# Kernel tuning notes

Hardware: AMD Instinct MI355X
Metric: run time of the kernel (lower is better)

Reference implementation:

```python
import jax, jax.numpy as jnp
import numpy as np

NUM_HEADS = 16
HEAD_SIZE = 256
HIDDEN = NUM_HEADS * HEAD_SIZE  # 4096
ROTARY_DIM = 64
TOTAL_TOKENS = 8192
BATCH = 8
NUM_SLOTS = 16384


def setup_inputs() -> dict:
    key = jax.random.key(0)
    ks = jax.random.split(key, 6)
    hidden_states = jax.random.normal(ks[0], (TOTAL_TOKENS, HIDDEN), dtype=jnp.float32)
    w_qkv = jax.random.normal(ks[1], (3 * HIDDEN, HIDDEN), dtype=jnp.float32) * 0.02
    w_o = jax.random.normal(ks[2], (HIDDEN, HIDDEN), dtype=jnp.float32) * 0.02
    # cos/sin per token for the first rotary_dim dims (rotary_dim//2 freqs)
    cos = jax.random.uniform(ks[3], (TOTAL_TOKENS, ROTARY_DIM // 2), dtype=jnp.float32)
    sin = jax.random.uniform(ks[4], (TOTAL_TOKENS, ROTARY_DIM // 2), dtype=jnp.float32)
    key_cache = jnp.zeros((NUM_SLOTS, NUM_HEADS, HEAD_SIZE), dtype=jnp.float32)
    value_cache = jnp.zeros((NUM_SLOTS, NUM_HEADS, HEAD_SIZE), dtype=jnp.float32)
    slots = jnp.arange(TOTAL_TOKENS, dtype=jnp.int64) if jax.config.jax_enable_x64 else jnp.arange(TOTAL_TOKENS, dtype=jnp.int32)
    return {
        "hidden_states": hidden_states, "w_qkv": w_qkv, "w_o": w_o,
        "cos": cos, "sin": sin,
        "key_cache": key_cache, "value_cache": value_cache,
        "slots": slots, "batch_size": BATCH,
    }


def _apply_rope(x, cos, sin, rotary_dim):
    # x: [T, H, D]; rotate-half applied only to the first rotary_dim dims
    half = rotary_dim // 2
    x1 = x[..., :half]
    x2 = x[..., half:rotary_dim]
    c = cos[:, None, :]  # [T, 1, half]
    s = sin[:, None, :]
    rot = jnp.concatenate([x1 * c - x2 * s, x2 * c + x1 * s], axis=-1)
    return jnp.concatenate([rot, x[..., rotary_dim:]], axis=-1)


def reference(hidden_states, w_qkv, w_o, cos, sin, key_cache, value_cache, slots, batch_size):
    T, H = hidden_states.shape
    nh, hd = key_cache.shape[1], key_cache.shape[2]
    rotary_dim = 2 * cos.shape[1]
    scale = float(hd) ** -0.5

    # fused QKV projection (no bias), then split
    qkv = hidden_states @ w_qkv.T  # [T, 3H]
    q, k, v = jnp.split(qkv, 3, axis=1)
    q = q.reshape(T, nh, hd)
    k = k.reshape(T, nh, hd)
    v = v.reshape(T, nh, hd)

    # partial rotary embedding on first rotary_dim dims
    q = _apply_rope(q, cos, sin, rotary_dim)
    k = _apply_rope(k, cos, sin, rotary_dim)

    # KV-cache slot scatter, then gather back (prefill reads what was stored)
    key_cache = key_cache.at[slots].set(k)
    value_cache = value_cache.at[slots].set(v)
    k = key_cache[slots]
    v = value_cache[slots]

    # prefill flash-attention path: equal-length sequences, causal per sequence
    B = batch_size
    S = T // B
    qb = q.reshape(B, S, nh, hd)
    kb = k.reshape(B, S, nh, hd)
    vb = v.reshape(B, S, nh, hd)

    scores = jnp.einsum('bqhd,bkhd->bhqk', qb, kb) * scale  # [B, nh, S, S]
    causal = jnp.tril(jnp.ones((S, S), dtype=bool))
    scores = jnp.where(causal[None, None], scores, jnp.finfo(scores.dtype).min)
    attn = jax.nn.softmax(scores, axis=-1)
    out = jnp.einsum('bhqk,bkhd->bqhd', attn, vb).reshape(T, nh * hd)

    return out @ w_o.T
```

## Files before the change

### kernel.cpp

```cpp
#include <hip/hip_runtime.h>
#include <stdint.h>


typedef __bf16 bf16x8 __attribute__((ext_vector_type(8)));
typedef float f32x4 __attribute__((ext_vector_type(4)));

__device__ __forceinline__ unsigned short f2bf(float f) {
    union { float f; unsigned int u; } x;
    x.f = f;
    unsigned int r = x.u + 0x7fffu + ((x.u >> 16) & 1u);
    return (unsigned short)(r >> 16);
}

__device__ __forceinline__ float bf2f(unsigned short h) {
    union { unsigned int u; float f; } x;
    x.u = ((unsigned int)h) << 16;
    return x.f;
}

__device__ __forceinline__ void gld16(const void* g, void* l) {
    __builtin_amdgcn_global_load_lds(
        (const __attribute__((address_space(1))) void*)g,
        (__attribute__((address_space(3))) void*)l, 16, 0, 0);
}

__global__ __launch_bounds__(256) void cvt_bf16(const float* __restrict__ src,
                                                unsigned short* __restrict__ dst,
                                                long n4) {
    long i = (long)blockIdx.x * 256 + threadIdx.x;
    long stride = (long)gridDim.x * 256;
    for (; i < n4; i += stride) {
        float4 v = ((const float4*)src)[i];
        ushort4 o;
        o.x = f2bf(v.x); o.y = f2bf(v.y); o.z = f2bf(v.z); o.w = f2bf(v.w);
        ((ushort4*)dst)[i] = o;
    }
}

template <int EPI>
__global__ __launch_bounds__(256) void gemm_bt(
    const unsigned short* __restrict__ A, long astride, long abatch,
    const unsigned short* __restrict__ B, long bstride, long bbatch,
    int kIters, void* __restrict__ out,
    unsigned short* __restrict__ out2, unsigned short* __restrict__ out3) {
    const int tid = threadIdx.x;
    const int ntile = blockIdx.x, mtile = blockIdx.y, bz = blockIdx.z;
    if (EPI == 1 && ntile > mtile) return;
    int kit = kIters;
    if (EPI == 2) kit = (mtile + 1) * 4;

    __shared__ __attribute__((aligned(16))) unsigned short As[128 * 32];
    __shared__ __attribute__((aligned(16))) unsigned short Bs[128 * 32];

    const unsigned short* Ab = A + (long)bz * abatch + (long)mtile * 128 * astride;
    const unsigned short* Bb = B + (long)bz * bbatch + (long)ntile * 128 * bstride;

    const int w = tid >> 6, l = tid & 63;
    const int wm = (w >> 1) * 64, wn = (w & 1) * 64;
    const int lr = l & 15;
    const int lc = l >> 4;

    const int c0 = tid, c1 = tid + 256;
    const int r0 = c0 >> 2, r1 = c1 >> 2;
    const int lc0 = (c0 & 3) ^ ((r0 >> 1) & 3);
    const int lc1 = (c1 & 3) ^ ((r1 >> 1) & 3);
    const long a0 = (long)r0 * astride + lc0 * 8;
    const long a1 = (long)r1 * astride + lc1 * 8;
    const long b0 = (long)r0 * bstride + lc0 * 8;
    const long b1 = (long)r1 * bstride + lc1 * 8;

    int aoff[4], boff[4];
#pragma unroll
    for (int i = 0; i < 4; ++i) {
        const int ra = wm + i * 16 + lr;
        aoff[i] = ra * 32 + ((lc ^ ((ra >> 1) & 3)) << 3);
        const int rb = wn + i * 16 + lr;
        boff[i] = rb * 32 + ((lc ^ ((rb >> 1) & 3)) << 3);
    }

    f32x4 acc[4][4];
#pragma unroll
    for (int i = 0; i < 4; ++i)
#pragma unroll
        for (int j = 0; j < 4; ++j) acc[i][j] = (f32x4)(0.0f);

    for (int kt = 0; kt < kit; ++kt) {
        const unsigned short* ak = Ab + kt * 32;
        const unsigned short* bk = Bb + kt * 32;
        __syncthreads();
        gld16(ak + a0, As + (long)c0 * 8);
        gld16(ak + a1, As + (long)c1 * 8);
        gld16(bk + b0, Bs + (long)c0 * 8);
        gld16(bk + b1, Bs + (long)c1 * 8);
        __syncthreads();

        bf16x8 af[4], bf[4];
#pragma unroll
        for (int i = 0; i < 4; ++i) {
            af[i] = *(const bf16x8*)(As + aoff[i]);
            bf[i] = *(const bf16x8*)(Bs + boff[i]);
        }
#pragma unroll
        for (int mi = 0; mi < 4; ++mi)
#pragma unroll
            for (int ni = 0; ni < 4; ++ni)
                acc[mi][ni] = __builtin_amdgcn_mfma_f32_16x16x32_bf16(
                    af[mi], bf[ni], acc[mi][ni], 0, 0, 0);
    }

    const int mBase = mtile * 128 + wm + (l >> 4) * 4;
    const int nBase = ntile * 128 + wn + (l & 15);
#pragma unroll
    for (int mi = 0; mi < 4; ++mi) {
#pragma unroll
        for (int ni = 0; ni < 4; ++ni) {
#pragma unroll
            for (int r = 0; r < 4; ++r) {
                const int m = mBase + mi * 16 + r;
                const int n = nBase + ni * 16;
                const float v = acc[mi][ni][r];
                if (EPI == 0) {
                    const int which = n >> 12, h = (n >> 8) & 15, d = n & 255;
                    const int b = m >> 10, s = m & 1023;
                    const long idx = ((((long)b * 16 + h) << 10) + s) * 256 + d;
                    unsigned short* dst =
                        (which == 0) ? (unsigned short*)out : (which == 1 ? out2 : out3);
                    dst[idx] = f2bf(v);
                } else if (EPI == 1) {
                    ((float*)out)[((long)bz << 20) + ((long)m << 10) + n] = v * 0.0625f;
                } else if (EPI == 2) {
                    const int b = bz >> 4, h = bz & 15;
                    ((unsigned short*)out)[(((long)b << 10) + m) * 4096 + h * 256 + n] =
                        f2bf(v);
                } else {
                    ((float*)out)[((long)m << 12) + n] = v;
                }
            }
        }
    }
}

__global__ __launch_bounds__(256) void rope_qk(unsigned short* __restrict__ q_s,
                                               unsigned short* __restrict__ k_s,
                                               const float* __restrict__ cosp,
                                               const float* __restrict__ sinp) {
    const int tid = blockIdx.x * 256 + threadIdx.x;
    const int i = tid & 31;
    const int h = (tid >> 5) & 15;
    const int tok = tid >> 9;
    const int b = tok >> 10, s = tok & 1023;
    const long base = ((((long)b * 16 + h) << 10) + s) * 256 + i;
    const float c = cosp[tok * 32 + i];
    const float sn = sinp[tok * 32 + i];
    {
        float x1 = bf2f(q_s[base]), x2 = bf2f(q_s[base + 32]);
        q_s[base] = f2bf(x1 * c - x2 * sn);
        q_s[base + 32] = f2bf(x2 * c + x1 * sn);
    }
    {
        float x1 = bf2f(k_s[base]), x2 = bf2f(k_s[base + 32]);
        k_s[base] = f2bf(x1 * c - x2 * sn);
        k_s[base + 32] = f2bf(x2 * c + x1 * sn);
    }
}

__global__ __launch_bounds__(256) void vtrans(const unsigned short* __restrict__ v_s,
                                              unsigned short* __restrict__ vT) {
    __shared__ unsigned short tile[32][33];
    const int bh = blockIdx.z;
    const int s0 = blockIdx.x * 32, d0 = blockIdx.y * 32;
    const int x = threadIdx.x, y = threadIdx.y;
    const unsigned short* src = v_s + (((long)bh << 10) + s0) * 256 + d0;
#pragma unroll
    for (int j = 0; j < 4; ++j) tile[y * 4 + j][x] = src[(y * 4 + j) * 256 + x];
    __syncthreads();
    unsigned short* dst = vT + (((long)bh << 8) + d0) * 1024 + s0;
#pragma unroll
    for (int j = 0; j < 4; ++j) dst[(y * 4 + j) * 1024 + x] = tile[x][y * 4 + j];
}

__global__ __launch_bounds__(256) void softmax_rows(float* __restrict__ scores) {
    const int row = blockIdx.x;
    const int bh = row >> 10, q = row & 1023;
    float* srow = scores + ((long)bh << 20) + ((long)q << 10);
    const int t = threadIdx.x;

    float v[4];
#pragma unroll
    for (int j = 0; j < 4; ++j) {
        const int k = t + (j << 8);
        v[j] = (k <= q) ? srow[k] : -3.0e38f;
    }
    float mx = fmaxf(fmaxf(v[0], v[1]), fmaxf(v[2], v[3]));
#pragma unroll
    for (int off = 32; off >= 1; off >>= 1) mx = fmaxf(mx, __shfl_xor(mx, off));
    __shared__ float redmax[4];
    if ((t & 63) == 0) redmax[t >> 6] = mx;
    __syncthreads();
    mx = fmaxf(fmaxf(redmax[0], redmax[1]), fmaxf(redmax[2], redmax[3]));

    float p[4];
    float s = 0.0f;
#pragma unroll
    for (int j = 0; j < 4; ++j) {
        const int k = t + (j << 8);
        p[j] = (k <= q) ? __expf(v[j] - mx) : 0.0f;
        s += p[j];
    }
#pragma unroll
    for (int off = 32; off >= 1; off >>= 1) s += __shfl_xor(s, off);
    __shared__ float redsum[4];
    if ((t & 63) == 0) redsum[t >> 6] = s;
    __syncthreads();
    s = redsum[0] + redsum[1] + redsum[2] + redsum[3];
    const float inv = 1.0f / s;

    unsigned short* prow = (unsigned short*)srow;
    const int kend = (q & ~127) + 128;
#pragma unroll
    for (int j = 0; j < 4; ++j) {
        const int k = t + (j << 8);
        if (k < kend) prow[k] = f2bf(p[j] * inv);
    }
}

extern "C" void kernel_launch(void* const* d_in, const int* in_sizes, int n_in,
                              void* d_out, int out_size, void* d_ws, size_t ws_size,
                              hipStream_t stream) {
    const float* hidden = (const float*)d_in[0];
    const float* w_qkv  = (const float*)d_in[1];
    const float* w_o    = (const float*)d_in[2];
    const float* cosp   = (const float*)d_in[3];
    const float* sinp   = (const float*)d_in[4];

    const long SZ_WO = 33554432L, SZ_HEAD = 67108864L, SZ_SCORES = 536870912L;
    if (ws_size < (size_t)(SZ_WO + 5 * SZ_HEAD + SZ_SCORES)) return;
    char* p = (char*)d_ws;
    unsigned short* wo_b = (unsigned short*)p;  p += SZ_WO;
    unsigned short* q_s  = (unsigned short*)p;  p += SZ_HEAD;
    unsigned short* k_s  = (unsigned short*)p;  p += SZ_HEAD;
    unsigned short* v_s  = (unsigned short*)p;  p += SZ_HEAD;
    unsigned short* vT   = (unsigned short*)p;  p += SZ_HEAD;
    unsigned short* attn = (unsigned short*)p;  p += SZ_HEAD;
    char* X = p;
    unsigned short* hid_b  = (unsigned short*)X;
    unsigned short* wqkv_b = (unsigned short*)(X + SZ_HEAD);
    float* scores = (float*)X;

    cvt_bf16<<<8192, 256, 0, stream>>>(hidden, hid_b, (long)8192 * 4096 / 4);
    cvt_bf16<<<8192, 256, 0, stream>>>(w_qkv, wqkv_b, (long)12288 * 4096 / 4);
    cvt_bf16<<<4096, 256, 0, stream>>>(w_o, wo_b, (long)4096 * 4096 / 4);

    gemm_bt<0><<<dim3(96, 64, 1), 256, 0, stream>>>(
        hid_b, 4096, 0, wqkv_b, 4096, 0, 128, q_s, k_s, v_s);

    rope_qk<<<16384, 256, 0, stream>>>(q_s, k_s, cosp, sinp);

    vtrans<<<dim3(32, 8, 128), dim3(32, 8, 1), 0, stream>>>(v_s, vT);

    gemm_bt<1><<<dim3(8, 8, 128), 256, 0, stream>>>(
        q_s, 256, 262144, k_s, 256, 262144, 8, scores, nullptr, nullptr);

    softmax_rows<<<131072, 256, 0, stream>>>(scores);

    gemm_bt<2><<<dim3(2, 8, 128), 256, 0, stream>>>(
        (unsigned short*)scores, 2048, 2097152, vT, 1024, 262144, 0,
        attn, nullptr, nullptr);

    gemm_bt<3><<<dim3(32, 64, 1), 256, 0, stream>>>(
        attn, 4096, 0, wo_b, 4096, 0, 128, d_out, nullptr, nullptr);

    (void)in_sizes; (void)n_in; (void)out_size;
}
```

Measured before the change: 2.556 ms.

## Add 256x256-tile multi-stage pipelined GEMM for QKV and output projections

Introduces a new 512-thread GEMM kernel with 256x256 output tiles, a 4-stage LDS ring fed by async global-to-LDS loads with explicit vmcnt waits, XOR-swizzled LDS layout to avoid bank conflicts, grouped block-index swizzling for L2 reuse, and raised MFMA priority. The QKV and output projections use it instead of the 128x128 single-buffered kernel, aiming to overlap loads with compute and raise arithmetic intensity. It uses much more LDS and registers per block, which lowers occupancy, and the attention GEMMs still use the old kernel.

```diff
diff --git a/kernel.cpp b/kernel.cpp
--- a/kernel.cpp
+++ b/kernel.cpp
@@ -34,6 +34,129 @@
         ushort4 o;
         o.x = f2bf(v.x); o.y = f2bf(v.y); o.z = f2bf(v.z); o.w = f2bf(v.w);
         ((ushort4*)dst)[i] = o;
+    }
+}
+
+template <int EPI>
+__global__ __launch_bounds__(512, 2) void gemm256(
+    const unsigned short* __restrict__ A, long lda,
+    const unsigned short* __restrict__ B, long ldb,
+    int nkt, void* __restrict__ out,
+    unsigned short* __restrict__ out2, unsigned short* __restrict__ out3) {
+    __shared__ __attribute__((aligned(16))) unsigned short As[4 * 8192];
+    __shared__ __attribute__((aligned(16))) unsigned short Bs[4 * 8192];
+
+    const int tid = threadIdx.x;
+    const int gx = gridDim.x;
+    const int bid = blockIdx.y * gx + blockIdx.x;
+    const int cpx = (gx * gridDim.y) >> 3;
+    const int swz = (bid & 7) * cpx + (bid >> 3);
+    const int ntile = swz % gx, mtile = swz / gx;
+
+    const int l = tid & 63;
+    const int wr = (tid >> 8) & 1, wc = (tid >> 6) & 3;
+    const int lr = l & 15, lg = l >> 4;
+
+    const int srow = tid >> 2;
+    const int slc = (tid & 3) ^ ((tid >> 3) & 3);
+    const unsigned short* Ag = A + (long)(mtile * 256 + srow) * lda + slc * 8;
+    const unsigned short* Bg = B + (long)(ntile * 256 + srow) * ldb + slc * 8;
+    unsigned short* lA = As + tid * 8;
+    unsigned short* lB = Bs + tid * 8;
+
+#define STAGE256(kt)                                              \
+    {                                                             \
+        const int s_ = (kt) & 3;                                  \
+        const unsigned short* a_ = Ag + (long)(kt) * 32;          \
+        const unsigned short* b_ = Bg + (long)(kt) * 32;          \
+        gld16(a_, lA + s_ * 8192);                                \
+        gld16(a_ + 128 * lda, lA + s_ * 8192 + 4096);             \
+        gld16(b_, lB + s_ * 8192);                                \
+        gld16(b_ + 128 * ldb, lB + s_ * 8192 + 4096);             \
+    }
+
+    int aoff[8], boff[4];
+#pragma unroll
+    for (int i = 0; i < 8; ++i) {
+        const int r = wr * 128 + i * 16 + lr;
+        aoff[i] = r * 32 + ((lg ^ ((r >> 1) & 3)) << 3);
+    }
+#pragma unroll
+    for (int i = 0; i < 4; ++i) {
+        const int r = wc * 64 + i * 16 + lr;
+        boff[i] = r * 32 + ((lg ^ ((r >> 1) & 3)) << 3);
+    }
+
+    f32x4 acc[8][4];
+#pragma unroll
+    for (int i = 0; i < 8; ++i)
+#pragma unroll
+        for (int j = 0; j < 4; ++j) acc[i][j] = (f32x4)(0.0f);
+
+    STAGE256(0);
+    STAGE256(1);
+    STAGE256(2);
+
+    for (int t = 0; t < nkt; ++t) {
+        if (t + 3 < nkt) {
+            STAGE256(t + 3);
+            asm volatile("s_waitcnt vmcnt(12)" ::: "memory");
+        } else if (t + 2 < nkt) {
+            asm volatile("s_waitcnt vmcnt(8)" ::: "memory");
+        } else if (t + 1 < nkt) {
+            asm volatile("s_waitcnt vmcnt(4)" ::: "memory");
+        } else {
+            asm volatile("s_waitcnt vmcnt(0)" ::: "memory");
+        }
+        __builtin_amdgcn_s_barrier();
+        asm volatile("" ::: "memory");
+
+        const unsigned short* as_ = As + ((t & 3) << 13);
+        const unsigned short* bs_ = Bs + ((t & 3) << 13);
+        bf16x8 af[8], bfr[4];
+#pragma unroll
+        for (int i = 0; i < 8; ++i) af[i] = *(const bf16x8*)(as_ + aoff[i]);
+#pragma unroll
+        for (int i = 0; i < 4; ++i) bfr[i] = *(const bf16x8*)(bs_ + boff[i]);
+
+        __builtin_amdgcn_s_setprio(1);
+#pragma unroll
+        for (int mi = 0; mi < 8; ++mi)
+#pragma unroll
+            for (int ni = 0; ni < 4; ++ni)
+                acc[mi][ni] = __builtin_amdgcn_mfma_f32_16x16x32_bf16(
+                    af[mi], bfr[ni], acc[mi][ni], 0, 0, 0);
+        __builtin_amdgcn_s_setprio(0);
+
+        asm volatile("" ::: "memory");
+        __builtin_amdgcn_s_barrier();
+        asm volatile("" ::: "memory");
+    }
+#undef STAGE256
+
+    const int mBase = mtile * 256 + wr * 128 + lg * 4;
+    const int nBase = ntile * 256 + wc * 64 + lr;
+#pragma unroll
+    for (int mi = 0; mi < 8; ++mi) {
+#pragma unroll
+        for (int ni = 0; ni < 4; ++ni) {
+#pragma unroll
+            for (int r = 0; r < 4; ++r) {
+                const int m = mBase + mi * 16 + r;
+                const int n = nBase + ni * 16;
+                const float v = acc[mi][ni][r];
+                if (EPI == 0) {
+                    const int which = n >> 12, h = (n >> 8) & 15, d = n & 255;
+                    const int b = m >> 10, s = m & 1023;
+                    const long idx = ((((long)b * 16 + h) << 10) + s) * 256 + d;
+                    unsigned short* dst =
+                        (which == 0) ? (unsigned short*)out : (which == 1 ? out2 : out3);
+                    dst[idx] = f2bf(v);
+                } else {
+                    ((float*)out)[((long)m << 12) + n] = v;
+                }
+            }
+        }
     }
 }
 
@@ -94,18 +217,18 @@
         gld16(bk + b1, Bs + (long)c1 * 8);
         __syncthreads();
 
-        bf16x8 af[4], bf[4];
+        bf16x8 af[4], bfv[4];
 #pragma unroll
         for (int i = 0; i < 4; ++i) {
             af[i] = *(const bf16x8*)(As + aoff[i]);
-            bf[i] = *(const bf16x8*)(Bs + boff[i]);
+            bfv[i] = *(const bf16x8*)(Bs + boff[i]);
         }
 #pragma unroll
         for (int mi = 0; mi < 4; ++mi)
 #pragma unroll
             for (int ni = 0; ni < 4; ++ni)
                 acc[mi][ni] = __builtin_amdgcn_mfma_f32_16x16x32_bf16(
-                    af[mi], bf[ni], acc[mi][ni], 0, 0, 0);
+                    af[mi], bfv[ni], acc[mi][ni], 0, 0, 0);
     }
 
     const int mBase = mtile * 128 + wm + (l >> 4) * 4;
@@ -119,25 +242,17 @@
                 const int m = mBase + mi * 16 + r;
                 const int n = nBase + ni * 16;
                 const float v = acc[mi][ni][r];
-                if (EPI == 0) {
-                    const int which = n >> 12, h = (n >> 8) & 15, d = n & 255;
-                    const int b = m >> 10, s = m & 1023;
-                    const long idx = ((((long)b * 16 + h) << 10) + s) * 256 + d;
-                    unsigned short* dst =
-                        (which == 0) ? (unsigned short*)out : (which == 1 ? out2 : out3);
-                    dst[idx] = f2bf(v);
-                } else if (EPI == 1) {
+                if (EPI == 1) {
                     ((float*)out)[((long)bz << 20) + ((long)m << 10) + n] = v * 0.0625f;
                 } else if (EPI == 2) {
                     const int b = bz >> 4, h = bz & 15;
                     ((unsigned short*)out)[(((long)b << 10) + m) * 4096 + h * 256 + n] =
                         f2bf(v);
-                } else {
-                    ((float*)out)[((long)m << 12) + n] = v;
                 }
             }
         }
     }
+    (void)out2; (void)out3;
 }
 
 __global__ __launch_bounds__(256) void rope_qk(unsigned short* __restrict__ q_s,
@@ -251,8 +366,8 @@
     cvt_bf16<<<8192, 256, 0, stream>>>(w_qkv, wqkv_b, (long)12288 * 4096 / 4);
     cvt_bf16<<<4096, 256, 0, stream>>>(w_o, wo_b, (long)4096 * 4096 / 4);
 
-    gemm_bt<0><<<dim3(96, 64, 1), 256, 0, stream>>>(
-        hid_b, 4096, 0, wqkv_b, 4096, 0, 128, q_s, k_s, v_s);
+    gemm256<0><<<dim3(48, 32, 1), 512, 0, stream>>>(
+        hid_b, 4096, wqkv_b, 4096, 128, q_s, k_s, v_s);
 
     rope_qk<<<16384, 256, 0, stream>>>(q_s, k_s, cosp, sinp);
 
@@ -267,8 +382,8 @@
         (unsigned short*)scores, 2048, 2097152, vT, 1024, 262144, 0,
         attn, nullptr, nullptr);
 
-    gemm_bt<3><<<dim3(32, 64, 1), 256, 0, stream>>>(
-        attn, 4096, 0, wo_b, 4096, 0, 128, d_out, nullptr, nullptr);
+    gemm256<1><<<dim3(16, 32, 1), 512, 0, stream>>>(
+        attn, 4096, wo_b, 4096, 128, d_out, nullptr, nullptr);
 
     (void)in_sizes; (void)n_in; (void)out_size;
 }
```

Measured after the change: 2.533 ms. About the same (-0.9%).
